# Optimization experiments

Hardware: AMD Instinct MI355X
Metric: run time of the kernel (lower is better)

## Reference

```python
import jax, jax.numpy as jnp
import numpy as np

B, H, T, D = 2, 16, 2048, 64
BASE_WINDOW = 256
FULL = 999999


def _make_window_sizes(num_heads=H, base_window=BASE_WINDOW):
    ws = []
    for h in range(num_heads):
        if h < num_heads // 4:
            ws.append(base_window)
        elif h < num_heads // 2:
            ws.append(base_window * 2)
        elif h < 3 * num_heads // 4:
            ws.append(base_window * 4)
        else:
            ws.append(FULL)
    return jnp.asarray(ws, dtype=jnp.int32)


def setup_inputs() -> dict:
    key = jax.random.key(0)
    kq, kk, kv = jax.random.split(key, 3)
    Q = jax.random.normal(kq, (B, H, T, D), dtype=jnp.float32)
    K = jax.random.normal(kk, (B, H, T, D), dtype=jnp.float32)
    V = jax.random.normal(kv, (B, H, T, D), dtype=jnp.float32)
    return {"Q": Q, "K": K, "V": V, "window_sizes": _make_window_sizes()}


def reference(Q, K, V, window_sizes):
    b, h, t, d = Q.shape
    scale = 1.0 / np.sqrt(d).astype(np.float32)
    idx = jnp.arange(t, dtype=jnp.int32)
    diff = idx[:, None] - idx[None, :]  # [T, T], q_idx - kv_idx
    # causal & |q-k| <= w  ==  0 <= diff <= w  (per head)
    mask = (diff >= 0) & (diff[None, :, :] <= window_sizes[:, None, None])  # [H, T, T]
    scores = jnp.einsum('bhqd,bhkd->bhqk', Q, K) * scale  # [B, H, T, T]
    scores = jnp.where(mask[None], scores, -jnp.inf)
    attn = jax.nn.softmax(scores, axis=-1)
    return jnp.einsum('bhqk,bhkd->bhqd', attn, V)
```

## Files before the change

kernel.cpp:

```cpp
#include <hip/hip_runtime.h>
#include <hip/hip_bf16.h>


constexpr int Bc = 2, Hc = 16, Tc = 2048, Dc = 64;
constexpr int BQ = 64;
constexpr int BK = 32;
constexpr float QSCALE = 0.125f * 1.44269504088896340736f;
constexpr float CMAX = 16.0f;

constexpr size_t KB_OFF = 256;
constexpr size_t VB_OFF = 256 + (size_t)Bc * Hc * Tc * Dc * 2;
constexpr int HEADE = Tc * Dc;

constexpr int KOFF = 0;
constexpr int VOFF = 8192;
constexpr int POFF = 18432;

typedef __attribute__((ext_vector_type(8))) short short8;
typedef __attribute__((ext_vector_type(4))) float float4v;

#if defined(__has_builtin)
#if __has_builtin(__builtin_amdgcn_exp2f)
#define EXP2 __builtin_amdgcn_exp2f
#endif
#endif
#ifndef EXP2
#define EXP2 exp2f
#endif

__device__ inline unsigned f2bf_u(float f) {
    union { float f; unsigned u; } v; v.f = f;
    return (v.u + 0x7fffu + ((v.u >> 16) & 1u)) >> 16;
}

__device__ inline short8 pack8(const float* t) {
    short8 r;
#pragma unroll
    for (int j = 0; j < 8; j++) r[j] = (short)f2bf_u(t[j]);
    return r;
}

__device__ inline unsigned pk_bf16(float a, float b) {
    __hip_bfloat162 h = __float22bfloat162_rn(make_float2(a, b));
    union { __hip_bfloat162 h; unsigned u; } v; v.h = h;
    return v.u;
}

__global__ __launch_bounds__(256)
void preconv_kernel(const float* __restrict__ K, const float* __restrict__ V,
                    unsigned short* __restrict__ Kb, unsigned short* __restrict__ Vtb) {
    const int blk = blockIdx.x;
    const int tid = threadIdx.x;
    if (blk < 2048) {
        const int base = blk * 2048 + tid * 8;
        float4v a = *(const float4v*)(K + base);
        float4v b = *(const float4v*)(K + base + 4);
        float t[8] = {a[0], a[1], a[2], a[3], b[0], b[1], b[2], b[3]};
        *(short8*)(Kb + base) = pack8(t);
    } else {
        __shared__ float tile[64][65];
        const int blk2 = blk - 2048;
        const int bh = blk2 >> 5;
        const int t0 = (blk2 & 31) * 64;
        const float* src = V + (size_t)bh * HEADE + (size_t)t0 * Dc;
#pragma unroll
        for (int i = 0; i < 4; i++) {
            const int r = (tid >> 4) + i * 16;
            const int d4 = (tid & 15) * 4;
            float4v v4 = *(const float4v*)(src + r * Dc + d4);
            tile[r][d4] = v4[0]; tile[r][d4 + 1] = v4[1];
            tile[r][d4 + 2] = v4[2]; tile[r][d4 + 3] = v4[3];
        }
        __syncthreads();
        unsigned short* dst = Vtb + (size_t)bh * HEADE + t0;
#pragma unroll
        for (int i = 0; i < 2; i++) {
            const int d = (tid >> 3) + 32 * i;
            const int c = tid & 7;
            float t[8];
#pragma unroll
            for (int j = 0; j < 8; j++) t[j] = tile[c * 8 + j][d];
            *(short8*)(dst + (size_t)d * Tc + c * 8) = pack8(t);
        }
    }
}

__global__ __launch_bounds__(256, 4)
void dswa_kernel(const float* __restrict__ Q,
                 const unsigned short* __restrict__ Kb,
                 const unsigned short* __restrict__ Vtb,
                 const int* __restrict__ wsz,
                 float* __restrict__ O) {
    __shared__ __align__(16) unsigned short LDS[20480];

    const int tid  = threadIdx.x;
    const int wave = tid >> 6;
    const int g    = wave >> 1;
    const int wq   = wave & 1;
    const int lane = tid & 63;
    const int quad = lane >> 4;
    const int l16  = lane & 15;
    const int ksw  = 0;  (void)ksw;
    const int psw  = (l16 & 3) << 3;

    unsigned short* Kg = &LDS[KOFF + g * 4096];
    unsigned short* Vg = &LDS[VOFF + g * 5120];
    unsigned short* Pl = &LDS[POFF + wave * 512];

    const int l128 = tid & 127;
    const int krow = l128 >> 2;
    const int kcol = (l128 & 3) * 16;
    const int vrow = l128 >> 1;
    const int vcol = (l128 & 1) * 16;

    const int blk = blockIdx.x;
    const int b  = blk & 1;
    const int qt = 31 - ((blk >> 1) & 31);
    const int h  = 15 - (blk >> 6);
    const int q0 = qt * BQ;
    const int win = wsz[h];

    const size_t headoff = (size_t)(b * Hc + h) * HEADE;
    const float* Qp = Q + headoff;
    const unsigned short* Kbh = Kb + headoff;
    const unsigned short* Vbh = Vtb + headoff;
    float* Op = O + headoff;

    short8 qf[2][2];
#pragma unroll
    for (int s = 0; s < 2; s++) {
        const int qrow = q0 + wq * 32 + s * 16 + l16;
#pragma unroll
        for (int c = 0; c < 2; c++) {
            const float* src = Qp + (size_t)qrow * Dc + c * 32 + quad * 8;
            float4v a = *(const float4v*)src;
            float4v d4 = *(const float4v*)(src + 4);
            float t[8] = {a[0]*QSCALE, a[1]*QSCALE, a[2]*QSCALE, a[3]*QSCALE,
                          d4[0]*QSCALE, d4[1]*QSCALE, d4[2]*QSCALE, d4[3]*QSCALE};
            qf[s][c] = pack8(t);
        }
    }

    float4v acc[2][4];
#pragma unroll
    for (int s = 0; s < 2; s++)
#pragma unroll
        for (int nb = 0; nb < 4; nb++) acc[s][nb] = (float4v){0.f, 0.f, 0.f, 0.f};
    float lp0 = 0.0f, lp1 = 0.0f;

    const int kv_lo = (max(0, q0 - win)) & ~(BK - 1);
    const int n_tiles = (q0 + BQ - kv_lo) >> 5;
    const int IT = (n_tiles + 1) >> 1;

    const int kv0g = kv_lo + g * BK;
    const unsigned short* kgp = Kbh + (size_t)(kv0g + krow) * Dc + kcol;
    const unsigned short* vgp = Vbh + (size_t)vrow * Tc + kv0g + vcol;

    short8 kr0, kr1, vr0, vr1;
    if (g < n_tiles) {
        kr0 = *(const short8*)(kgp);
        kr1 = *(const short8*)(kgp + 8);
        vr0 = *(const short8*)(vgp);
        vr1 = *(const short8*)(vgp + 8);
    }
    kgp += 64 * Dc; vgp += 64;

    for (int t = 0; t < IT; ++t) {
        const int ti = g + 2 * t;
        const bool act = ti < n_tiles;
        const int kv0 = kv_lo + ti * BK;
        unsigned short* Kl = Kg + (t & 1) * 2048;
        unsigned short* Vt = Vg + (t & 1) * 2560;

        if (act) {
            const int ks = (krow & 7) << 3;
            *(short8*)&Kl[krow * 64 + (kcol ^ ks)] = kr0;
            *(short8*)&Kl[krow * 64 + ((kcol + 8) ^ ks)] = kr1;
            *(short8*)&Vt[vrow * 40 + vcol] = vr0;
            *(short8*)&Vt[vrow * 40 + vcol + 8] = vr1;
        }
        __syncthreads();

        if (ti + 2 < n_tiles) {
            kr0 = *(const short8*)(kgp);
            kr1 = *(const short8*)(kgp + 8);
            vr0 = *(const short8*)(vgp);
            vr1 = *(const short8*)(vgp + 8);
        }
        kgp += 64 * Dc; vgp += 64;

        if (act) {
            float4v sT0[2], sT1[2];
#pragma unroll
            for (int mb = 0; mb < 2; mb++) {
                float4v c0 = {-CMAX, -CMAX, -CMAX, -CMAX};
                float4v c1 = {-CMAX, -CMAX, -CMAX, -CMAX};
#pragma unroll
                for (int ch = 0; ch < 2; ch++) {
                    const int row = mb * 16 + l16;
                    short8 kf = *(short8*)&Kl[row * 64 +
                                              ((ch * 32 + quad * 8) ^ ((row & 7) << 3))];
                    c0 = __builtin_amdgcn_mfma_f32_16x16x32_bf16(kf, qf[0][ch], c0, 0, 0, 0);
                    c1 = __builtin_amdgcn_mfma_f32_16x16x32_bf16(kf, qf[1][ch], c1, 0, 0, 0);
                }
                sT0[mb] = c0; sT1[mb] = c1;
            }

            short8 pf0, pf1;
            {
                const int rs = q0 + wq * 32;
                const bool interior = (kv0 + 31 <= rs) && (rs + 15 - kv0 <= win);
                if (!interior) {
                    const int dbase = rs + l16 - kv0 - quad * 4;
#pragma unroll
                    for (int mb = 0; mb < 2; mb++)
#pragma unroll
                        for (int r = 0; r < 4; r++) {
                            const unsigned diff = (unsigned)(dbase - mb * 16 - r);
                            sT0[mb][r] = (diff <= (unsigned)win) ? sT0[mb][r] : -3.0e38f;
                        }
                }
#pragma unroll
                for (int mb = 0; mb < 2; mb++) {
                    float p0 = EXP2(sT0[mb][0]);
                    float p1 = EXP2(sT0[mb][1]);
                    float p2 = EXP2(sT0[mb][2]);
                    float p3 = EXP2(sT0[mb][3]);
                    lp0 += (p0 + p1) + (p2 + p3);
                    unsigned* dst = (unsigned*)&Pl[l16 * 32 + ((mb * 16 + quad * 4) ^ psw)];
                    dst[0] = pk_bf16(p0, p1);
                    dst[1] = pk_bf16(p2, p3);
                }
                __asm__ volatile("" ::: "memory");
                pf0 = *(short8*)&Pl[l16 * 32 + ((quad * 8) ^ psw)];
            }
            {
                const int rs = q0 + wq * 32 + 16;
                const bool interior = (kv0 + 31 <= rs) && (rs + 15 - kv0 <= win);
                if (!interior) {
                    const int dbase = rs + l16 - kv0 - quad * 4;
#pragma unroll
                    for (int mb = 0; mb < 2; mb++)
#pragma unroll
                        for (int r = 0; r < 4; r++) {
                            const unsigned diff = (unsigned)(dbase - mb * 16 - r);
                            sT1[mb][r] = (diff <= (unsigned)win) ? sT1[mb][r] : -3.0e38f;
                        }
                }
                __asm__ volatile("" ::: "memory");
#pragma unroll
                for (int mb = 0; mb < 2; mb++) {
                    float p0 = EXP2(sT1[mb][0]);
                    float p1 = EXP2(sT1[mb][1]);
                    float p2 = EXP2(sT1[mb][2]);
                    float p3 = EXP2(sT1[mb][3]);
                    lp1 += (p0 + p1) + (p2 + p3);
                    unsigned* dst = (unsigned*)&Pl[l16 * 32 + ((mb * 16 + quad * 4) ^ psw)];
                    dst[0] = pk_bf16(p0, p1);
                    dst[1] = pk_bf16(p2, p3);
                }
                __asm__ volatile("" ::: "memory");
                pf1 = *(short8*)&Pl[l16 * 32 + ((quad * 8) ^ psw)];
            }

#pragma unroll
            for (int nb = 0; nb < 4; nb++) {
                short8 vf = *(short8*)&Vt[(nb * 16 + l16) * 40 + quad * 8];
                acc[0][nb] = __builtin_amdgcn_mfma_f32_16x16x32_bf16(pf0, vf, acc[0][nb], 0, 0, 0);
                acc[1][nb] = __builtin_amdgcn_mfma_f32_16x16x32_bf16(pf1, vf, acc[1][nb], 0, 0, 0);
            }
        }
    }

    lp0 += __shfl_xor(lp0, 16); lp0 += __shfl_xor(lp0, 32);
    lp1 += __shfl_xor(lp1, 16); lp1 += __shfl_xor(lp1, 32);

    __syncthreads();
    float* fl = (float*)LDS;
    if (g == 1) {
#pragma unroll
        for (int s = 0; s < 2; s++) {
            if (quad == 0) fl[(wq * 32 + s * 16 + l16) * 66 + 64] = (s ? lp1 : lp0);
#pragma unroll
            for (int r = 0; r < 4; r++) {
                const int row = wq * 32 + s * 16 + quad * 4 + r;
#pragma unroll
                for (int nb = 0; nb < 4; nb++)
                    fl[row * 66 + nb * 16 + l16] = acc[s][nb][r];
            }
        }
    }
    __syncthreads();
    if (g == 0) {
#pragma unroll
        for (int s = 0; s < 2; s++) {
            const float lps = s ? lp1 : lp0;
#pragma unroll
            for (int r = 0; r < 4; r++) {
                const int row = wq * 32 + s * 16 + quad * 4 + r;
                const float l0 = __shfl(lps, quad * 4 + r);
                const float lt = l0 + fl[row * 66 + 64];
                const float inv = 1.0f / lt;
                float* dst = Op + (size_t)(q0 + row) * Dc;
#pragma unroll
                for (int nb = 0; nb < 4; nb++)
                    dst[nb * 16 + l16] = (acc[s][nb][r] + fl[row * 66 + nb * 16 + l16]) * inv;
            }
        }
    }
}

extern "C" void kernel_launch(void* const* d_in, const int* in_sizes, int n_in,
                              void* d_out, int out_size, void* d_ws, size_t ws_size,
                              hipStream_t stream) {
    (void)in_sizes; (void)n_in; (void)ws_size; (void)out_size;
    const float* Q = (const float*)d_in[0];
    const float* K = (const float*)d_in[1];
    const float* V = (const float*)d_in[2];
    const int* wsz = (const int*)d_in[3];
    float* Out = (float*)d_out;

    unsigned short* Kb  = (unsigned short*)((char*)d_ws + KB_OFF);
    unsigned short* Vtb = (unsigned short*)((char*)d_ws + VB_OFF);

    preconv_kernel<<<dim3(3072), dim3(256), 0, stream>>>(K, V, Kb, Vtb);
    dswa_kernel<<<dim3(1024), dim3(256), 0, stream>>>(Q, Kb, Vtb, wsz, Out);
}
```

Baseline: 125.7 us.

## Fuse K/V bf16 preconversion into attention kernel with per-head atomic barrier

```diff
diff --git a/kernel.cpp b/kernel.cpp
--- a/kernel.cpp
+++ b/kernel.cpp
@@ -46,51 +46,15 @@
     return v.u;
 }
 
-__global__ __launch_bounds__(256)
-void preconv_kernel(const float* __restrict__ K, const float* __restrict__ V,
-                    unsigned short* __restrict__ Kb, unsigned short* __restrict__ Vtb) {
-    const int blk = blockIdx.x;
-    const int tid = threadIdx.x;
-    if (blk < 2048) {
-        const int base = blk * 2048 + tid * 8;
-        float4v a = *(const float4v*)(K + base);
-        float4v b = *(const float4v*)(K + base + 4);
-        float t[8] = {a[0], a[1], a[2], a[3], b[0], b[1], b[2], b[3]};
-        *(short8*)(Kb + base) = pack8(t);
-    } else {
-        __shared__ float tile[64][65];
-        const int blk2 = blk - 2048;
-        const int bh = blk2 >> 5;
-        const int t0 = (blk2 & 31) * 64;
-        const float* src = V + (size_t)bh * HEADE + (size_t)t0 * Dc;
-#pragma unroll
-        for (int i = 0; i < 4; i++) {
-            const int r = (tid >> 4) + i * 16;
-            const int d4 = (tid & 15) * 4;
-            float4v v4 = *(const float4v*)(src + r * Dc + d4);
-            tile[r][d4] = v4[0]; tile[r][d4 + 1] = v4[1];
-            tile[r][d4 + 2] = v4[2]; tile[r][d4 + 3] = v4[3];
-        }
-        __syncthreads();
-        unsigned short* dst = Vtb + (size_t)bh * HEADE + t0;
-#pragma unroll
-        for (int i = 0; i < 2; i++) {
-            const int d = (tid >> 3) + 32 * i;
-            const int c = tid & 7;
-            float t[8];
-#pragma unroll
-            for (int j = 0; j < 8; j++) t[j] = tile[c * 8 + j][d];
-            *(short8*)(dst + (size_t)d * Tc + c * 8) = pack8(t);
-        }
-    }
-}
-
 __global__ __launch_bounds__(256, 4)
 void dswa_kernel(const float* __restrict__ Q,
-                 const unsigned short* __restrict__ Kb,
-                 const unsigned short* __restrict__ Vtb,
+                 const float* __restrict__ Kf,
+                 const float* __restrict__ Vf,
                  const int* __restrict__ wsz,
-                 float* __restrict__ O) {
+                 float* __restrict__ O,
+                 unsigned* __restrict__ headctr,
+                 unsigned short* __restrict__ Kb,
+                 unsigned short* __restrict__ Vtb) {
     __shared__ __align__(16) unsigned short LDS[20480];
 
     const int tid  = threadIdx.x;
@@ -100,7 +64,6 @@
     const int lane = tid & 63;
     const int quad = lane >> 4;
     const int l16  = lane & 15;
-    const int ksw  = 0;  (void)ksw;
     const int psw  = (l16 & 3) << 3;
 
     unsigned short* Kg = &LDS[KOFF + g * 4096];
@@ -119,12 +82,51 @@
     const int h  = 15 - (blk >> 6);
     const int q0 = qt * BQ;
     const int win = wsz[h];
-
-    const size_t headoff = (size_t)(b * Hc + h) * HEADE;
+    const int bh = b * Hc + h;
+
+    const size_t headoff = (size_t)bh * HEADE;
     const float* Qp = Q + headoff;
-    const unsigned short* Kbh = Kb + headoff;
-    const unsigned short* Vbh = Vtb + headoff;
+    unsigned short* Kbh = Kb + headoff;
+    unsigned short* Vbh = Vtb + headoff;
     float* Op = O + headoff;
+
+    {
+        const float* ks = Kf + headoff + (size_t)q0 * Dc;
+        unsigned short* kd = Kbh + (size_t)q0 * Dc;
+        const int r = tid >> 2;
+        const int c = (tid & 3) * 16;
+        {
+            const float* s = ks + r * Dc + c;
+            float t0[8], t1[8];
+#pragma unroll
+            for (int j = 0; j < 8; j++) { t0[j] = s[j]; t1[j] = s[8 + j]; }
+            *(short8*)(kd + r * Dc + c) = pack8(t0);
+            *(short8*)(kd + r * Dc + c + 8) = pack8(t1);
+        }
+        float* tile = (float*)LDS;
+        const float* vs = Vf + headoff + (size_t)q0 * Dc;
+#pragma unroll
+        for (int i = 0; i < 4; i++) {
+            const int rr = (tid >> 4) + i * 16;
+            const int d4 = (tid & 15) * 4;
+            float4v v4 = *(const float4v*)(vs + rr * Dc + d4);
+            tile[rr * 65 + d4] = v4[0]; tile[rr * 65 + d4 + 1] = v4[1];
+            tile[rr * 65 + d4 + 2] = v4[2]; tile[rr * 65 + d4 + 3] = v4[3];
+        }
+        __syncthreads();
+#pragma unroll
+        for (int i = 0; i < 2; i++) {
+            const int d = (tid >> 3) + 32 * i;
+            const int cc = tid & 7;
+            float t[8];
+#pragma unroll
+            for (int j = 0; j < 8; j++) t[j] = tile[(cc * 8 + j) * 65 + d];
+            *(short8*)(Vbh + (size_t)d * Tc + q0 + cc * 8) = pack8(t);
+        }
+        __syncthreads();
+        __threadfence();
+        if (tid == 0) atomicAdd(&headctr[bh], 1u);
+    }
 
     short8 qf[2][2];
 #pragma unroll
@@ -140,6 +142,13 @@
             qf[s][c] = pack8(t);
         }
     }
+
+    if (tid == 0) {
+        while (atomicAdd(&headctr[bh], 0u) < 32u)
+            __builtin_amdgcn_s_sleep(8);
+    }
+    __syncthreads();
+    __threadfence();
 
     float4v acc[2][4];
 #pragma unroll
@@ -320,9 +329,11 @@
     const int* wsz = (const int*)d_in[3];
     float* Out = (float*)d_out;
 
+    unsigned* headctr = (unsigned*)d_ws;
     unsigned short* Kb  = (unsigned short*)((char*)d_ws + KB_OFF);
     unsigned short* Vtb = (unsigned short*)((char*)d_ws + VB_OFF);
 
-    preconv_kernel<<<dim3(3072), dim3(256), 0, stream>>>(K, V, Kb, Vtb);
-    dswa_kernel<<<dim3(1024), dim3(256), 0, stream>>>(Q, Kb, Vtb, wsz, Out);
-}
+    hipMemsetAsync(headctr, 0, 128, stream);
+    dswa_kernel<<<dim3(1024), dim3(256), 0, stream>>>(Q, K, V, wsz, Out,
+                                                      headctr, Kb, Vtb);
+}
```

Measured after the change: 411.8 us. 3.28x slower.
